# Optimization experiments

Measured on AMD Instinct MI355X. Metric: run time of the kernel, lower is better.

## Reference

```python
import jax, jax.numpy as jnp
import numpy as np

N_NODES = 100000
N_EDGES = 1600000
F_IN, HID, N_CLS = 64, 64, 40
K = 3  # Chebyshev order


def setup_inputs() -> dict:
    key = jax.random.key(0)
    k = jax.random.split(key, 7)
    x = jax.random.normal(k[0], (N_NODES, F_IN), dtype=jnp.float32)
    edge_index = jax.random.randint(k[1], (2, N_EDGES), 0, N_NODES, dtype=jnp.int32)
    W1 = jax.random.normal(k[2], (K, F_IN, HID), dtype=jnp.float32) * 0.05
    b1 = jax.random.normal(k[3], (HID,), dtype=jnp.float32) * 0.05
    W2 = jax.random.normal(k[4], (K, HID, N_CLS), dtype=jnp.float32) * 0.05
    b2 = jax.random.normal(k[5], (N_CLS,), dtype=jnp.float32) * 0.05
    return {"x": x, "edge_index": edge_index, "W1": W1, "b1": b1, "W2": W2, "b2": b2}


def _norm(edge_index, n):
    # PyG ChebConv with sym normalization and lambda_max=2.0:
    # L_hat edge weight = -deg^{-1/2}[src] * deg^{-1/2}[dst]; self-loop weight 0.
    src, dst = edge_index[0], edge_index[1]
    keep = (src != dst).astype(jnp.float32)  # remove_self_loops
    deg = jax.ops.segment_sum(keep, src, num_segments=n)
    dis = jnp.where(deg > 0, 1.0 / jnp.sqrt(jnp.maximum(deg, 1.0)), 0.0)
    w = -dis[src] * dis[dst] * keep
    return src, dst, w


def _spmm(x, src, dst, w, n):
    # out[i] = sum_{e: dst[e]==i} w[e] * x[src[e]]
    return jax.ops.segment_sum(w[:, None] * x[src], dst, num_segments=n)


def _cheb_conv(x, src, dst, w, W, b, n):
    Tx0 = x
    out = Tx0 @ W[0]
    Tx1 = _spmm(x, src, dst, w, n)
    out = out + Tx1 @ W[1]
    for k in range(2, W.shape[0]):
        Tx2 = 2.0 * _spmm(Tx1, src, dst, w, n) - Tx0
        out = out + Tx2 @ W[k]
        Tx0, Tx1 = Tx1, Tx2
    return out + b


def reference(x, edge_index, W1, b1, W2, b2):
    n = x.shape[0]
    src, dst, w = _norm(edge_index, n)
    h = jax.nn.relu(_cheb_conv(x, src, dst, w, W1, b1, n))
    out = _cheb_conv(h, src, dst, w, W2, b2, n)
    return jax.nn.softmax(out, axis=1)
```

## Files before the change

### kernel.cpp

```cpp
#include <hip/hip_runtime.h>
#include <hip/hip_fp16.h>

#define N_NODES 100000
#define N_EDGES 1600000
#define NCLS 40
#define NBUCK 196
#define CAPE 8960
#define CAPC 10752
#define DUMMY N_NODES

typedef unsigned short u16;
typedef unsigned int u32;
typedef short bf16x8 __attribute__((ext_vector_type(8)));
typedef float f32x4 __attribute__((ext_vector_type(4)));

static inline size_t align256(size_t x) { return (x + 255) & ~(size_t)255; }

__device__ __forceinline__ float bf2f(u16 h) { return __uint_as_float(((u32)h) << 16); }
__device__ __forceinline__ u16 f2bf(float f) {
    u32 u = __float_as_uint(f);
    u += 0x7FFFu + ((u >> 16) & 1u);
    return (u16)(u >> 16);
}
__device__ __forceinline__ u32 pk2(u16 a, u16 b) { return (u32)a | ((u32)b << 16); }
__device__ __forceinline__ u32 pack15(float f) {
    return ((u32)__half_as_ushort(__float2half(f))) & 0x7FFFu;
}
__device__ __forceinline__ float unpack15(u32 bits) {
    return __half2float(__ushort_as_half((u16)bits));
}
__device__ __forceinline__ float blo(u32 v) { return __uint_as_float(v << 16); }
__device__ __forceinline__ float bhi(u32 v) { return __uint_as_float(v & 0xFFFF0000u); }

#define PS_BLOCKS 391
#define CONV_BLOCKS 6250

__global__ __launch_bounds__(256) void pscatter_conv(const int* __restrict__ src,
                                                     const int* __restrict__ dst,
                                                     int* __restrict__ gFillD,
                                                     int* __restrict__ gFillS,
                                                     u32* __restrict__ partD,
                                                     u16* __restrict__ partS,
                                                     const float* __restrict__ x,
                                                     u16* __restrict__ xb) {
    if (blockIdx.x >= PS_BLOCKS) {
        int i = (blockIdx.x - PS_BLOCKS) * 256 + threadIdx.x;
        float4 v = *(const float4*)(x + (size_t)i * 4);
        ushort4 o;
        o.x = f2bf(v.x); o.y = f2bf(v.y); o.z = f2bf(v.z); o.w = f2bf(v.w);
        *(ushort4*)(xb + (size_t)i * 4) = o;
        return;
    }
    __shared__ int histD[NBUCK], histS[NBUCK], chunkD[NBUCK], chunkS[NBUCK];
    int tid = threadIdx.x;
    int base = blockIdx.x * 4096;

    int4 sv[4], dv[4];
#pragma unroll
    for (int j = 0; j < 4; ++j) {
        int idx = base + j * 1024 + tid * 4;
        if (idx < N_EDGES) {
            sv[j] = *(const int4*)(src + idx);
            dv[j] = *(const int4*)(dst + idx);
        } else {
            sv[j] = make_int4(0, 0, 0, 0);
            dv[j] = make_int4(0, 0, 0, 0);
        }
    }

    for (int i = tid; i < NBUCK; i += 256) { histD[i] = 0; histS[i] = 0; }
    __syncthreads();
#pragma unroll
    for (int j = 0; j < 4; ++j)
#pragma unroll
        for (int k = 0; k < 4; ++k) {
            int s = ((const int*)&sv[j])[k], d = ((const int*)&dv[j])[k];
            if (s != d) {
                atomicAdd(&histD[d >> 9], 1);
                atomicAdd(&histS[s >> 9], 1);
            }
        }
    __syncthreads();
    for (int B = tid; B < NBUCK; B += 256) {
        int cD = histD[B];
        chunkD[B] = cD ? atomicAdd(&gFillD[B], cD) : 0;
        int cS = histS[B];
        chunkS[B] = cS ? atomicAdd(&gFillS[B], cS) : 0;
    }
    __syncthreads();
    for (int i = tid; i < NBUCK; i += 256) { histD[i] = 0; histS[i] = 0; }
    __syncthreads();
#pragma unroll
    for (int j = 0; j < 4; ++j)
#pragma unroll
        for (int k = 0; k < 4; ++k) {
            int s = ((const int*)&sv[j])[k], d = ((const int*)&dv[j])[k];
            if (s != d) {
                int bD = d >> 9;
                int r = atomicAdd(&histD[bD], 1);
                int o = chunkD[bD] + r;
                if (o < CAPE) partD[bD * CAPE + o] = ((u32)s << 9) | (u32)(d & 511);
                int bS = s >> 9;
                int r2 = atomicAdd(&histS[bS], 1);
                int o2 = chunkS[bS] + r2;
                if (o2 < CAPE) partS[bS * CAPE + o2] = (u16)(s & 511);
            }
        }
}

__global__ __launch_bounds__(256) void build_dis(const u16* __restrict__ partS,
                                                 const int* __restrict__ gFillS,
                                                 float* __restrict__ dis) {
    __shared__ int cnt[512];
    int tid = threadIdx.x;
    int B = blockIdx.x;
    for (int i = tid; i < 512; i += 256) cnt[i] = 0;
    __syncthreads();
    int nS = min(gFillS[B], CAPE);
    for (int i = tid; i < nS; i += 256) atomicAdd(&cnt[partS[B * CAPE + i]], 1);
    __syncthreads();
    for (int n = tid; n < 512; n += 256) {
        int node = B * 512 + n;
        if (node < N_NODES) {
            int dg = cnt[n];
            dis[node] = dg > 0 ? 1.0f / sqrtf((float)dg) : 0.0f;
        }
    }
}

__global__ __launch_bounds__(256) void build_csr(const u32* __restrict__ partD,
                                                 const int* __restrict__ gFillD,
                                                 const float* __restrict__ dis,
                                                 u32* __restrict__ csr,
                                                 int2* __restrict__ meta) {
    __shared__ int cnt[512], loc[512], rnk[512];
    int tid = threadIdx.x;
    int B = blockIdx.x;
    for (int i = tid; i < 512; i += 256) { cnt[i] = 0; rnk[i] = 0; }
    __syncthreads();
    int nD = min(gFillD[B], CAPE);
    for (int i = tid; i < nD; i += 256) atomicAdd(&cnt[partD[B * CAPE + i] & 511], 1);
    __syncthreads();
    if (tid < 64) {
        int bb = tid * 8, c8[8], mysum = 0;
#pragma unroll
        for (int j = 0; j < 8; ++j) { c8[j] = (cnt[bb + j] + 7) & ~7; mysum += c8[j]; }
        int incl = mysum;
#pragma unroll
        for (int off = 1; off < 64; off <<= 1) {
            int v = __shfl_up(incl, off);
            if (tid >= off) incl += v;
        }
        int run = incl - mysum;
#pragma unroll
        for (int j = 0; j < 8; ++j) { loc[bb + j] = run; run += c8[j]; }
    }
    __syncthreads();
    for (int n = tid; n < 512; n += 256) {
        int node = B * 512 + n;
        if (node < N_NODES) {
            int c = cnt[n], c8 = (c + 7) & ~7;
            meta[node] = make_int2(B * CAPC + loc[n], c);
            for (int e = c; e < c8; ++e) csr[B * CAPC + loc[n] + e] = (u32)DUMMY;
        }
    }
    for (int i = tid; i < nD; i += 256) {
        u32 p = partD[B * CAPE + i];
        int ln = p & 511;
        u32 s = p >> 9;
        int r = atomicAdd(&rnk[ln], 1);
        int pos = loc[ln] + r;
        if (pos < CAPC) csr[B * CAPC + pos] = s | (pack15(dis[s]) << 17);
    }
}

template <int J>
__device__ __forceinline__ void edge_step(u32 ent, const uint4* __restrict__ in4,
                                          int p, float* a) {
    u32 q = (u32)__builtin_amdgcn_ds_swizzle((int)ent, (J << 5) | 0x18);
    u32 s = q & 0x1FFFFu;
    float w = unpack15(q >> 17);
    uint4 v = in4[((size_t)s << 3) + p];
    a[0] = fmaf(w, blo(v.x), a[0]);
    a[1] = fmaf(w, bhi(v.x), a[1]);
    a[2] = fmaf(w, blo(v.y), a[2]);
    a[3] = fmaf(w, bhi(v.y), a[3]);
    a[4] = fmaf(w, blo(v.z), a[4]);
    a[5] = fmaf(w, bhi(v.z), a[5]);
    a[6] = fmaf(w, blo(v.w), a[6]);
    a[7] = fmaf(w, bhi(v.w), a[7]);
}

#define SPMM_BLOCKS 3125

__global__ __launch_bounds__(256) void spmm(const u16* __restrict__ in,
                                            const float* __restrict__ dis,
                                            const int2* __restrict__ meta,
                                            const u32* __restrict__ csr,
                                            u16* __restrict__ outhi) {
    const int tid = threadIdx.x;
    const int lane = tid & 63;
    const int gw = blockIdx.x * 4 + (tid >> 6);
    const int node = gw * 8 + (lane >> 3);
    const int p = lane & 7;

    int2 mt = meta[node];
    int c8 = (mt.y + 7) & ~7;
    const u32* lst = csr + mt.x;
    const uint4* in4 = (const uint4*)in;

    float a[8] = {0.f, 0.f, 0.f, 0.f, 0.f, 0.f, 0.f, 0.f};

    for (int e = 0; e < c8; e += 8) {
        u32 ent = lst[e + p];
        edge_step<0>(ent, in4, p, a);
        edge_step<1>(ent, in4, p, a);
        edge_step<2>(ent, in4, p, a);
        edge_step<3>(ent, in4, p, a);
        edge_step<4>(ent, in4, p, a);
        edge_step<5>(ent, in4, p, a);
        edge_step<6>(ent, in4, p, a);
        edge_step<7>(ent, in4, p, a);
    }

    float vd = -dis[node];
    uint4 H;
    H.x = pk2(f2bf(vd * a[0]), f2bf(vd * a[1]));
    H.y = pk2(f2bf(vd * a[2]), f2bf(vd * a[3]));
    H.z = pk2(f2bf(vd * a[4]), f2bf(vd * a[5]));
    H.w = pk2(f2bf(vd * a[6]), f2bf(vd * a[7]));
    *((uint4*)((u32*)outhi + (((size_t)node << 5) + (p << 2)))) = H;
}

#define DGRID 1250
#define DNT 5
#define LSTR 200
#define LSTR2 72

__device__ __forceinline__ float foldW(const float* __restrict__ W, int kk, int col,
                                       int ncols) {
    float wv = W[kk * ncols + col];
    if (kk < 64) wv -= W[(kk + 128) * ncols + col];
    else if (kk >= 128) wv += wv;
    return wv;
}

__global__ __launch_bounds__(256) void dense1_mf(const float* __restrict__ x,
                                                 const u16* __restrict__ a1h,
                                                 const u16* __restrict__ tyh,
                                                 const float* __restrict__ W,
                                                 const float* __restrict__ bias,
                                                 u16* __restrict__ ohi,
                                                 u16* __restrict__ olo) {
    __shared__ u16 Ah[16 * LSTR], Al[16 * LSTR2];
    const int tid = threadIdx.x, wid = tid >> 6, lane = tid & 63;
    const int lrow = lane & 15, lk8 = (lane >> 4) * 8;
    const int col = wid * 16 + lrow;

    bf16x8 wh[6], wl[6];
#pragma unroll
    for (int c = 0; c < 6; ++c) {
        bf16x8 h, l;
#pragma unroll
        for (int i = 0; i < 8; ++i) {
            float wv = foldW(W, c * 32 + lk8 + i, col, 64);
            u16 hb_ = f2bf(wv);
            h[i] = (short)hb_;
            l[i] = (short)f2bf(wv - bf2f(hb_));
        }
        wh[c] = h; wl[c] = l;
    }
    float bv = bias[col];
    const int srow = tid >> 4, sc4 = (tid & 15) * 4;

    for (int t = 0; t < DNT; ++t) {
        int r0 = (blockIdx.x * DNT + t) * 16;
        size_t rb = ((size_t)(r0 + srow) << 6) + sc4;
        {
            float4 v = *(const float4*)&x[rb];
            const float* vp = (const float*)&v;
            ushort4 hv, lv;
#pragma unroll
            for (int i = 0; i < 4; ++i) {
                u16 hb_ = f2bf(vp[i]);
                ((u16*)&hv)[i] = hb_;
                ((u16*)&lv)[i] = f2bf(vp[i] - bf2f(hb_));
            }
            *(ushort4*)&Ah[srow * LSTR + sc4] = hv;
            *(ushort4*)&Al[srow * LSTR2 + sc4] = lv;
        }
        *(ushort4*)&Ah[srow * LSTR + 64 + sc4] = *(const ushort4*)&a1h[rb];
        *(ushort4*)&Ah[srow * LSTR + 128 + sc4] = *(const ushort4*)&tyh[rb];
        __syncthreads();

        f32x4 acc = {bv, bv, bv, bv};
#pragma unroll
        for (int c = 0; c < 6; ++c) {
            bf16x8 ah = *(const bf16x8*)&Ah[lrow * LSTR + c * 32 + lk8];
            acc = __builtin_amdgcn_mfma_f32_16x16x32_bf16(ah, wh[c], acc, 0, 0, 0);
            acc = __builtin_amdgcn_mfma_f32_16x16x32_bf16(ah, wl[c], acc, 0, 0, 0);
        }
#pragma unroll
        for (int c = 0; c < 2; ++c) {
            bf16x8 al = *(const bf16x8*)&Al[lrow * LSTR2 + c * 32 + lk8];
            acc = __builtin_amdgcn_mfma_f32_16x16x32_bf16(al, wh[c], acc, 0, 0, 0);
        }
        __syncthreads();

#pragma unroll
        for (int j = 0; j < 4; ++j) {
            int row = r0 + (lane >> 4) * 4 + j;
            float v = fmaxf(acc[j], 0.0f);
            u16 hb_ = f2bf(v);
            ohi[((size_t)row << 6) + col] = hb_;
            olo[((size_t)row << 6) + col] = f2bf(v - bf2f(hb_));
        }
    }
}

__global__ __launch_bounds__(256) void dense2_mf(const u16* __restrict__ a0h,
                                                 const u16* __restrict__ a0l,
                                                 const u16* __restrict__ a1h,
                                                 const u16* __restrict__ tyh,
                                                 const float* __restrict__ W,
                                                 const float* __restrict__ bias,
                                                 float* __restrict__ out) {
    __shared__ u16 Ah[16 * LSTR], Al[16 * LSTR2];
    __shared__ float Ls[16][48];
    const int tid = threadIdx.x, wid = tid >> 6, lane = tid & 63;
    const int lrow = lane & 15, lk8 = (lane >> 4) * 8;
    const int col = wid * 16 + lrow;
    const bool act = (wid < 3);
    const bool cok = act && (col < NCLS);

    bf16x8 wh[6], wl[6];
#pragma unroll
    for (int c = 0; c < 6; ++c) {
        bf16x8 h = 0, l = 0;
        if (cok) {
#pragma unroll
            for (int i = 0; i < 8; ++i) {
                float wv = foldW(W, c * 32 + lk8 + i, col, NCLS);
                u16 hb_ = f2bf(wv);
                h[i] = (short)hb_;
                l[i] = (short)f2bf(wv - bf2f(hb_));
            }
        }
        wh[c] = h; wl[c] = l;
    }
    float bv = cok ? bias[col] : 0.0f;
    const int srow = tid >> 4, sc4 = (tid & 15) * 4;

    for (int t = 0; t < DNT; ++t) {
        int r0 = (blockIdx.x * DNT + t) * 16;
        size_t rb = ((size_t)(r0 + srow) << 6) + sc4;
        *(ushort4*)&Ah[srow * LSTR + sc4] = *(const ushort4*)&a0h[rb];
        *(ushort4*)&Al[srow * LSTR2 + sc4] = *(const ushort4*)&a0l[rb];
        *(ushort4*)&Ah[srow * LSTR + 64 + sc4] = *(const ushort4*)&a1h[rb];
        *(ushort4*)&Ah[srow * LSTR + 128 + sc4] = *(const ushort4*)&tyh[rb];
        __syncthreads();

        if (act) {
            f32x4 acc = {bv, bv, bv, bv};
#pragma unroll
            for (int c = 0; c < 6; ++c) {
                bf16x8 ah = *(const bf16x8*)&Ah[lrow * LSTR + c * 32 + lk8];
                acc = __builtin_amdgcn_mfma_f32_16x16x32_bf16(ah, wh[c], acc, 0, 0, 0);
                acc = __builtin_amdgcn_mfma_f32_16x16x32_bf16(ah, wl[c], acc, 0, 0, 0);
            }
#pragma unroll
            for (int c = 0; c < 2; ++c) {
                bf16x8 al = *(const bf16x8*)&Al[lrow * LSTR2 + c * 32 + lk8];
                acc = __builtin_amdgcn_mfma_f32_16x16x32_bf16(al, wh[c], acc, 0, 0, 0);
            }
#pragma unroll
            for (int j = 0; j < 4; ++j) Ls[(lane >> 4) * 4 + j][col] = acc[j];
        }
        __syncthreads();

        {
            int row = wid * 4 + (lane >> 4);
            int cg = lane & 15;
            float v0 = Ls[row][cg];
            float v1 = Ls[row][cg + 16];
            float v2 = (cg < 8) ? Ls[row][cg + 32] : -1e30f;
            float m = fmaxf(fmaxf(v0, v1), v2);
#pragma unroll
            for (int o = 8; o; o >>= 1) m = fmaxf(m, __shfl_xor(m, o));
            float e0 = expf(v0 - m), e1 = expf(v1 - m);
            float e2 = (cg < 8) ? expf(v2 - m) : 0.0f;
            float s = e0 + e1 + e2;
#pragma unroll
            for (int o = 8; o; o >>= 1) s += __shfl_xor(s, o);
            float inv = 1.0f / s;
            size_t ob = (size_t)(r0 + row) * NCLS;
            out[ob + cg] = e0 * inv;
            out[ob + cg + 16] = e1 * inv;
            if (cg < 8) out[ob + cg + 32] = e2 * inv;
        }
    }
}


extern "C" void kernel_launch(void* const* d_in, const int* in_sizes, int n_in,
                              void* d_out, int out_size, void* d_ws, size_t ws_size,
                              hipStream_t stream) {
    const float* x = (const float*)d_in[0];
    const int* edge_index = (const int*)d_in[1];
    const float* W1 = (const float*)d_in[2];
    const float* b1 = (const float*)d_in[3];
    const float* W2 = (const float*)d_in[4];
    const float* b2 = (const float*)d_in[5];
    float* out = (float*)d_out;

    const int* src = edge_index;
    const int* dst = edge_index + N_EDGES;

    char* ws = (char*)d_ws;
    size_t off = 0;
    auto carve = [&](size_t bytes) -> void* {
        void* p = ws + off;
        off = align256(off + bytes);
        return p;
    };
    int* gFillD = (int*)carve((size_t)NBUCK * 4);
    int* gFillS = (int*)carve((size_t)NBUCK * 4);
    size_t zero_bytes = off;
    u32* partD = (u32*)carve((size_t)NBUCK * CAPE * 4);
    u16* partS = (u16*)carve((size_t)NBUCK * CAPE * 2);
    u32* csr = (u32*)carve((size_t)NBUCK * CAPC * 4 + 1024);
    int2* meta = (int2*)carve((size_t)N_NODES * 8);
    float* dis = (float*)carve((size_t)(N_NODES + 1) * 4);
    const size_t FB = (size_t)(N_NODES + 1) * 64 * 2;
    u16* xb  = (u16*)carve(FB);
    u16* t1h = (u16*)carve(FB);
    u16* tyh = (u16*)carve(FB);
    u16* hh  = (u16*)carve(FB);
    u16* hl  = (u16*)carve(FB);

    (void)hipMemsetAsync(d_ws, 0, zero_bytes, stream);

    pscatter_conv<<<PS_BLOCKS + CONV_BLOCKS, 256, 0, stream>>>(src, dst, gFillD, gFillS,
                                                               partD, partS, x, xb);
    build_dis<<<NBUCK, 256, 0, stream>>>(partS, gFillS, dis);
    build_csr<<<NBUCK, 256, 0, stream>>>(partD, gFillD, dis, csr, meta);

    spmm<<<SPMM_BLOCKS, 256, 0, stream>>>(xb, dis, meta, csr, t1h);
    spmm<<<SPMM_BLOCKS, 256, 0, stream>>>(t1h, dis, meta, csr, tyh);
    dense1_mf<<<DGRID, 256, 0, stream>>>(x, t1h, tyh, W1, b1, hh, hl);

    spmm<<<SPMM_BLOCKS, 256, 0, stream>>>(hh, dis, meta, csr, t1h);
    spmm<<<SPMM_BLOCKS, 256, 0, stream>>>(t1h, dis, meta, csr, tyh);
    dense2_mf<<<DGRID, 256, 0, stream>>>(hh, hl, t1h, tyh, W2, b2, out);
}
```

Baseline: 222.7 us.

## Bin nodes by padded degree and reorder SpMM work for wavefront balance

Builds a degree-bin histogram in build_csr, computes bin offsets, and scatters node ids into an order array sorted by padded degree bucket. The SpMM kernel reads its node from this order, so the 8 nodes sharing a wavefront have similar edge counts, which cuts divergence and idle lanes in the per-wave edge loop. The cost is two extra small kernels plus one indirection load per node. Output writes now go to scattered node positions, which can hurt write and gather locality.

```diff
diff --git a/kernel.cpp b/kernel.cpp
--- a/kernel.cpp
+++ b/kernel.cpp
@@ -132,10 +132,13 @@
                                                  const int* __restrict__ gFillD,
                                                  const float* __restrict__ dis,
                                                  u32* __restrict__ csr,
-                                                 int2* __restrict__ meta) {
+                                                 int2* __restrict__ meta,
+                                                 int* __restrict__ binCnt) {
     __shared__ int cnt[512], loc[512], rnk[512];
+    __shared__ int binh[8];
     int tid = threadIdx.x;
     int B = blockIdx.x;
+    if (tid < 8) binh[tid] = 0;
     for (int i = tid; i < 512; i += 256) { cnt[i] = 0; rnk[i] = 0; }
     __syncthreads();
     int nD = min(gFillD[B], CAPE);
@@ -162,6 +165,7 @@
             int c = cnt[n], c8 = (c + 7) & ~7;
             meta[node] = make_int2(B * CAPC + loc[n], c);
             for (int e = c; e < c8; ++e) csr[B * CAPC + loc[n] + e] = (u32)DUMMY;
+            atomicAdd(&binh[min(c8 >> 3, 7)], 1);
         }
     }
     for (int i = tid; i < nD; i += 256) {
@@ -171,6 +175,47 @@
         int r = atomicAdd(&rnk[ln], 1);
         int pos = loc[ln] + r;
         if (pos < CAPC) csr[B * CAPC + pos] = s | (pack15(dis[s]) << 17);
+    }
+    __syncthreads();
+    if (tid < 8 && binh[tid] > 0) atomicAdd(&binCnt[tid], binh[tid]);
+}
+
+__global__ void prefix8(const int* __restrict__ binCnt, int* __restrict__ binBase) {
+    if (threadIdx.x == 0) {
+        int run = 0;
+        for (int b = 0; b < 8; ++b) { binBase[b] = run; run += binCnt[b]; }
+    }
+}
+
+__global__ __launch_bounds__(256) void order_scatter(const int2* __restrict__ meta,
+                                                     const int* __restrict__ binBase,
+                                                     int* __restrict__ binFill,
+                                                     int* __restrict__ order) {
+    __shared__ int lcnt[8], chunk[8], lrank[8];
+    int tid = threadIdx.x, B = blockIdx.x;
+    if (tid < 8) { lcnt[tid] = 0; lrank[tid] = 0; }
+    __syncthreads();
+    int bins[2];
+#pragma unroll
+    for (int k = 0; k < 2; ++k) {
+        int node = B * 512 + tid + k * 256;
+        if (node < N_NODES) {
+            int c8 = (meta[node].y + 7) & ~7;
+            int b = min(c8 >> 3, 7);
+            bins[k] = b;
+            atomicAdd(&lcnt[b], 1);
+        } else bins[k] = -1;
+    }
+    __syncthreads();
+    if (tid < 8) chunk[tid] = lcnt[tid] ? atomicAdd(&binFill[tid], lcnt[tid]) : 0;
+    __syncthreads();
+#pragma unroll
+    for (int k = 0; k < 2; ++k) {
+        if (bins[k] >= 0) {
+            int node = B * 512 + tid + k * 256;
+            int r = atomicAdd(&lrank[bins[k]], 1);
+            order[binBase[bins[k]] + chunk[bins[k]] + r] = node;
+        }
     }
 }
 
@@ -197,11 +242,13 @@
                                             const float* __restrict__ dis,
                                             const int2* __restrict__ meta,
                                             const u32* __restrict__ csr,
+                                            const int* __restrict__ order,
                                             u16* __restrict__ outhi) {
     const int tid = threadIdx.x;
     const int lane = tid & 63;
     const int gw = blockIdx.x * 4 + (tid >> 6);
-    const int node = gw * 8 + (lane >> 3);
+    const int slot = gw * 8 + (lane >> 3);
+    const int node = order[slot];
     const int p = lane & 7;
 
     int2 mt = meta[node];
@@ -425,7 +472,11 @@
     };
     int* gFillD = (int*)carve((size_t)NBUCK * 4);
     int* gFillS = (int*)carve((size_t)NBUCK * 4);
+    int* binCnt = (int*)carve(8 * 4);
+    int* binFill = (int*)carve(8 * 4);
     size_t zero_bytes = off;
+    int* binBase = (int*)carve(8 * 4);
+    int* order = (int*)carve((size_t)N_NODES * 4);
     u32* partD = (u32*)carve((size_t)NBUCK * CAPE * 4);
     u16* partS = (u16*)carve((size_t)NBUCK * CAPE * 2);
     u32* csr = (u32*)carve((size_t)NBUCK * CAPC * 4 + 1024);
@@ -443,13 +494,15 @@
     pscatter_conv<<<PS_BLOCKS + CONV_BLOCKS, 256, 0, stream>>>(src, dst, gFillD, gFillS,
                                                                partD, partS, x, xb);
     build_dis<<<NBUCK, 256, 0, stream>>>(partS, gFillS, dis);
-    build_csr<<<NBUCK, 256, 0, stream>>>(partD, gFillD, dis, csr, meta);
-
-    spmm<<<SPMM_BLOCKS, 256, 0, stream>>>(xb, dis, meta, csr, t1h);
-    spmm<<<SPMM_BLOCKS, 256, 0, stream>>>(t1h, dis, meta, csr, tyh);
+    build_csr<<<NBUCK, 256, 0, stream>>>(partD, gFillD, dis, csr, meta, binCnt);
+    prefix8<<<1, 64, 0, stream>>>(binCnt, binBase);
+    order_scatter<<<NBUCK, 256, 0, stream>>>(meta, binBase, binFill, order);
+
+    spmm<<<SPMM_BLOCKS, 256, 0, stream>>>(xb, dis, meta, csr, order, t1h);
+    spmm<<<SPMM_BLOCKS, 256, 0, stream>>>(t1h, dis, meta, csr, order, tyh);
     dense1_mf<<<DGRID, 256, 0, stream>>>(x, t1h, tyh, W1, b1, hh, hl);
 
-    spmm<<<SPMM_BLOCKS, 256, 0, stream>>>(hh, dis, meta, csr, t1h);
-    spmm<<<SPMM_BLOCKS, 256, 0, stream>>>(t1h, dis, meta, csr, tyh);
+    spmm<<<SPMM_BLOCKS, 256, 0, stream>>>(hh, dis, meta, csr, order, t1h);
+    spmm<<<SPMM_BLOCKS, 256, 0, stream>>>(t1h, dis, meta, csr, order, tyh);
     dense2_mf<<<DGRID, 256, 0, stream>>>(hh, hl, t1h, tyh, W2, b2, out);
 }
```

New measurement: 234.0 us. +5.1%, slower.
